# Kernel tuning notes

Measured on AMD Instinct MI355X. Metric: run time of the kernel, lower is better.

## Reference

```python
import jax, jax.numpy as jnp
import numpy as np

H = 8
DK = 32  # head_dim = 256 // 8
SCALE = 1.0 / np.float32(np.sqrt(DK))
EPS = 1e-5


def _ln(x, g, b):
    mu = jnp.mean(x, axis=-1, keepdims=True)
    var = jnp.var(x, axis=-1, keepdims=True)
    return (x - mu) / jnp.sqrt(var + EPS) * g + b


def _lin(x, W, b):
    return x @ W + b


def setup_inputs() -> dict:
    key = jax.random.key(0)
    ks = jax.random.split(key, 16)
    B, M, N, D, F = 4, 64, 512, 256, 1024
    s = 0.02
    inp = {
        "machine_emb": jax.random.normal(ks[0], (B, M, D), jnp.float32),
        "op_emb": jax.random.normal(ks[1], (B, N, D), jnp.float32),
        "edge_emb": jax.random.normal(ks[2], (B, N, M, D), jnp.float32),
        "o2m_mask": jax.random.bernoulli(ks[3], 0.3, (B, N, M)),
    }
    # projection weights stored as (in, out)
    for i, nm in enumerate(["q", "k", "v", "o", "ks", "vs", "e"]):
        inp["W" + nm] = jax.random.normal(ks[4 + i], (D, D), jnp.float32) * s
        inp["b" + nm] = jnp.zeros((D,), jnp.float32)
    # layernorms: norm1 (g1/b1), norm2 (g2/b2), norm_op (gop/bop)
    for nm in ["1", "2", "op"]:
        inp["g" + nm] = jnp.ones((D,), jnp.float32)
        inp["bn" + nm] = jnp.zeros((D,), jnp.float32)
    # FFN
    inp["Wf1"] = jax.random.normal(ks[11], (D, F), jnp.float32) * s
    inp["bf1"] = jnp.zeros((F,), jnp.float32)
    inp["Wf2"] = jax.random.normal(ks[12], (F, D), jnp.float32) * s
    inp["bf2"] = jnp.zeros((D,), jnp.float32)
    return inp


def reference(machine_emb, op_emb, edge_emb, o2m_mask,
              Wq, bq, Wk, bk, Wv, bv, Wo, bo, Wks, bks, Wvs, bvs, We, be,
              g1, bn1, g2, bn2, gop, bnop, Wf1, bf1, Wf2, bf2):
    B, M, D = machine_emb.shape
    N = op_emb.shape[1]

    residual = machine_emb
    machine_norm = _ln(machine_emb, g1, bn1)
    op_norm = _ln(op_emb, gop, bnop)

    # (B, H, M, dk) / (B, H, N, dk)
    q_m = _lin(machine_norm, Wq, bq).reshape(B, M, H, DK).transpose(0, 2, 1, 3)
    k_o = _lin(op_norm, Wk, bk).reshape(B, N, H, DK).transpose(0, 2, 1, 3)
    v_o = _lin(op_norm, Wv, bv).reshape(B, N, H, DK).transpose(0, 2, 1, 3)

    # edge: (B,N,M,D) -> (B,H,M,N,dk)
    edge = _lin(edge_emb, We, be).reshape(B, N, M, H, DK)
    edge = edge.transpose(0, 3, 2, 1, 4)  # bhmnd

    q_total = q_m[:, :, :, None, :] + edge          # (B,H,M,N,dk)
    k_total = k_o[:, :, None, :, :] + edge          # (B,H,M,N,dk)
    v_total = v_o[:, :, None, :, :] + edge          # (B,H,M,N,dk)

    scores = jnp.sum(q_total * k_total, axis=-1) * SCALE  # (B,H,M,N)

    k_self = _lin(machine_norm, Wks, bks).reshape(B, M, H, DK).transpose(0, 2, 1, 3)
    self_scores = jnp.sum(q_m * k_self, axis=-1) * SCALE   # (B,H,M)

    cross_mask = o2m_mask.transpose(0, 2, 1)[:, None, :, :]  # (B,1,M,N)
    combined_scores = jnp.concatenate([self_scores[..., None], scores], axis=-1)  # (B,H,M,1+N)
    self_flag = jnp.ones((B, 1, M, 1), dtype=bool)
    combined_mask = jnp.concatenate([self_flag, jnp.broadcast_to(cross_mask, (B, 1, M, N))], axis=-1)
    combined_scores = jnp.where(combined_mask, combined_scores, -jnp.inf)

    attn = jax.nn.softmax(combined_scores, axis=-1)
    attn = jnp.where(jnp.isnan(attn), 0.0, attn)

    v_self = _lin(machine_norm, Wvs, bvs).reshape(B, M, H, DK).transpose(0, 2, 1, 3)
    combined_values = jnp.concatenate([v_self[:, :, :, None, :], v_total], axis=3)  # (B,H,M,1+N,dk)

    attn_out = jnp.einsum('bhmi,bhmid->bhmd', attn, combined_values)
    attn_out = attn_out.transpose(0, 2, 1, 3).reshape(B, M, D)
    attn_out = _lin(attn_out, Wo, bo)

    machine_emb = residual + attn_out
    h = _ln(machine_emb, g2, bn2)
    ffn = _lin(jax.nn.relu(_lin(h, Wf1, bf1)), Wf2, bf2)
    return machine_emb + ffn
```

## Files before the change

### kernel.cpp

```cpp
#include <hip/hip_runtime.h>
#include <hip/hip_bf16.h>
#include <math.h>

#define H_ 8
#define DK_ 32
#define B_ 4
#define M_ 64
#define N_ 512
#define D_ 256
#define F_ 1024

static constexpr float SCALE = 0.17677669529663687f;
static constexpr float EPS = 1e-5f;

typedef __bf16 bf16x8 __attribute__((ext_vector_type(8)));
typedef float f32x4 __attribute__((ext_vector_type(4)));

__device__ inline float bfbits2f(unsigned int b) {
    union { unsigned int i; float f; } c; c.i = b << 16; return c.f;
}
__device__ inline void unpack8(uint4 u, float* f) {
    f[0] = bfbits2f(u.x & 0xffffu); f[1] = bfbits2f(u.x >> 16);
    f[2] = bfbits2f(u.y & 0xffffu); f[3] = bfbits2f(u.y >> 16);
    f[4] = bfbits2f(u.z & 0xffffu); f[5] = bfbits2f(u.z >> 16);
    f[6] = bfbits2f(u.w & 0xffffu); f[7] = bfbits2f(u.w >> 16);
}

__global__ __launch_bounds__(256) void detect_kernel(const unsigned int* __restrict__ mask,
                                                     int* __restrict__ flags) {
    __shared__ int s2[256];
    int t = threadIdx.x;
    int cgt = 0;
    for (int i = 0; i < 128; ++i) {
        unsigned int w = mask[t * 128 + i];
        if (w > 1u) cgt++;
    }
    s2[t] = cgt;
    __syncthreads();
    if (t == 0) {
        int b = 0;
        for (int i = 0; i < 256; ++i) b += s2[i];
        flags[1] = (b > 0) ? 1 : 0;
    }
}

struct TTArgs {
    const void* src[9];
    void* dst[9];
    int tcum[9];
    int kl[9];
    int nl[9];
};

__global__ __launch_bounds__(256) void prep_transpose(TTArgs a) {
    __shared__ float ld[64][65];
    int bx = blockIdx.x;
    int ti = 0;
    while (bx >= a.tcum[ti]) ti++;
    int j = bx - (ti ? a.tcum[ti - 1] : 0);
    int K = 1 << a.kl[ti], N = 1 << a.nl[ti];
    int ntn = N >> 6;
    int kt = j / ntn, nt = j - kt * ntn;
    const float* src = (const float*)a.src[ti];
    __hip_bfloat16* dst = (__hip_bfloat16*)a.dst[ti];
    int t = threadIdx.x;
    int col = t & 63, r0 = t >> 6;
#pragma unroll
    for (int i = 0; i < 16; ++i) {
        int r = i * 4 + r0;
        ld[r][col] = src[(size_t)(kt * 64 + r) * N + nt * 64 + col];
    }
    __syncthreads();
#pragma unroll
    for (int i = 0; i < 16; ++i) {
        int r = i * 4 + r0;
        dst[(size_t)(nt * 64 + r) * K + kt * 64 + col] = __float2bfloat16(ld[col][r]);
    }
}

__global__ __launch_bounds__(256) void prep_bias(const float* bq, const float* bks,
                                                 const float* bvs, const float* bk,
                                                 const float* bv,
                                                 float* bqksvs, float* bkv) {
    int t = threadIdx.x;
    bqksvs[t] = bq[t];
    bqksvs[256 + t] = bks[t];
    bqksvs[512 + t] = bvs[t];
    bkv[t] = bk[t];
    bkv[256 + t] = bv[t];
}

__device__ inline float block_reduce256(float v, bool is_max, float* sbuf) {
#pragma unroll
    for (int off = 32; off > 0; off >>= 1) {
        float o = __shfl_down(v, off, 64);
        v = is_max ? fmaxf(v, o) : (v + o);
    }
    int lane = threadIdx.x & 63, wid = threadIdx.x >> 6;
    if (lane == 0) sbuf[wid] = v;
    __syncthreads();
    float r;
    if (is_max) r = fmaxf(fmaxf(sbuf[0], sbuf[1]), fmaxf(sbuf[2], sbuf[3]));
    else        r = sbuf[0] + sbuf[1] + sbuf[2] + sbuf[3];
    __syncthreads();
    return r;
}

__global__ __launch_bounds__(256) void ln_kernel(const float* __restrict__ xin,
                                                 const float* __restrict__ g,
                                                 const float* __restrict__ bta,
                                                 __hip_bfloat16* __restrict__ out) {
    __shared__ float sbuf[4];
    int row = blockIdx.x, d = threadIdx.x;
    size_t idx = (size_t)row * 256 + d;
    float x = xin[idx];
    float s  = block_reduce256(x, false, sbuf);
    float ss = block_reduce256(x * x, false, sbuf);
    float mu = s * (1.f / 256.f);
    float var = ss * (1.f / 256.f) - mu * mu;
    float y = (x - mu) * rsqrtf(var + EPS) * g[d] + bta[d];
    out[idx] = __float2bfloat16(y);
}

__global__ __launch_bounds__(256) void gemm64(const __hip_bfloat16* __restrict__ A,
                                              const __hip_bfloat16* __restrict__ BT,
                                              const float* __restrict__ bias,
                                              const float* __restrict__ resid,
                                              void* __restrict__ out,
                                              int K, int ldc, int flags) {
    __shared__ __align__(16) __bf16 As[64 * 40];
    __shared__ __align__(16) __bf16 Bs[64 * 40];
    const int rowBase = blockIdx.x * 64;
    const int colBase = blockIdx.y * 64;
    const int t = threadIdx.x;
    const int w = t >> 6;
    const int l = t & 63;
    const int lrow = l & 15;
    const int lk8 = (l >> 4) * 8;
    const int ar = t >> 2;
    const int ac = (t & 3) * 8;

    f32x4 acc[4] = {};
    for (int k0 = 0; k0 < K; k0 += 32) {
        bf16x8 av = *(const bf16x8*)(A + (size_t)(rowBase + ar) * K + k0 + ac);
        bf16x8 bv = *(const bf16x8*)(BT + (size_t)(colBase + ar) * K + k0 + ac);
        __syncthreads();
        *(bf16x8*)(As + ar * 40 + ac) = av;
        *(bf16x8*)(Bs + ar * 40 + ac) = bv;
        __syncthreads();
        bf16x8 af = *(const bf16x8*)(As + (w * 16 + lrow) * 40 + lk8);
#pragma unroll
        for (int c = 0; c < 4; ++c) {
            bf16x8 bf = *(const bf16x8*)(Bs + (c * 16 + lrow) * 40 + lk8);
            acc[c] = __builtin_amdgcn_mfma_f32_16x16x32_bf16(af, bf, acc[c], 0, 0, 0);
        }
    }
    int rbase = rowBase + w * 16 + ((l >> 4) * 4);
#pragma unroll
    for (int c = 0; c < 4; ++c) {
        int col = colBase + c * 16 + (l & 15);
        float bb = bias[col];
#pragma unroll
        for (int r = 0; r < 4; ++r) {
            int row = rbase + r;
            size_t oi = (size_t)row * ldc + col;
            float v = acc[c][r] + bb;
            if (flags & 1) v = fmaxf(v, 0.f);
            if (flags & 4) v += resid[oi];
            if (flags & 8) ((float*)out)[oi] = v;
            else ((__hip_bfloat16*)out)[oi] = __float2bfloat16(v);
        }
    }
}

__global__ __launch_bounds__(256) void edge_gemm4(const float* __restrict__ E,
                                                  const __hip_bfloat16* __restrict__ WeT,
                                                  const float* __restrict__ be,
                                                  const __hip_bfloat16* __restrict__ qkvs,
                                                  const __hip_bfloat16* __restrict__ kov,
                                                  const void* __restrict__ mask,
                                                  const int* __restrict__ flags,
                                                  __hip_bfloat16* __restrict__ eperm,
                                                  float* __restrict__ scBn) {
    __shared__ __align__(16) __bf16 smem[64 * 272];
    __bf16* As = smem;
    __bf16* Cs = smem;
    const int bn = blockIdx.x;
    const int b = bn >> 9, n = bn & 511;
    const int t = threadIdx.x;
    const int w = t >> 6;
    const int l = t & 63;
    const int lrow = l & 15;
    const int lk8 = (l >> 4) * 8;
    const int ar = t >> 2;
    const int ac = (t & 3) * 8;
    const float* Ab = E + (size_t)bn * 64 * 256;

    f32x4 acc[4][4] = {};
    for (int k0 = 0; k0 < 256; k0 += 32) {
        const float* ap = Ab + (size_t)ar * 256 + k0 + ac;
        float4 x0 = *(const float4*)ap;
        float4 x1 = *(const float4*)(ap + 4);
        bf16x8 av;
        av[0] = (__bf16)x0.x; av[1] = (__bf16)x0.y; av[2] = (__bf16)x0.z; av[3] = (__bf16)x0.w;
        av[4] = (__bf16)x1.x; av[5] = (__bf16)x1.y; av[6] = (__bf16)x1.z; av[7] = (__bf16)x1.w;
        __syncthreads();
        *(bf16x8*)(As + ar * 40 + ac) = av;
        __syncthreads();
        bf16x8 af[4];
#pragma unroll
        for (int rr = 0; rr < 4; ++rr)
            af[rr] = *(const bf16x8*)(As + (rr * 16 + lrow) * 40 + lk8);
#pragma unroll
        for (int c = 0; c < 4; ++c) {
            bf16x8 bf = *(const bf16x8*)(WeT + (size_t)(w * 64 + c * 16 + lrow) * 256 + k0 + lk8);
#pragma unroll
            for (int rr = 0; rr < 4; ++rr)
                acc[rr][c] = __builtin_amdgcn_mfma_f32_16x16x32_bf16(af[rr], bf, acc[rr][c], 0, 0, 0);
        }
    }
    __syncthreads();
#pragma unroll
    for (int c = 0; c < 4; ++c) {
        int col = w * 64 + c * 16 + (l & 15);
        float bb = be[col];
#pragma unroll
        for (int rr = 0; rr < 4; ++rr) {
#pragma unroll
            for (int r = 0; r < 4; ++r) {
                int m = rr * 16 + (l >> 4) * 4 + r;
                Cs[m * 272 + col] = (__bf16)(acc[rr][c][r] + bb);
            }
        }
    }
    __syncthreads();
    const bool u8 = flags[1] != 0;
    const int seg = t & 31;
    const int h = seg >> 2;
    const int dk8 = (seg & 3) * 8;
#pragma unroll
    for (int j = 0; j < 8; ++j) {
        int m = j * 8 + (t >> 5);
        uint4 ev4 = *(const uint4*)(Cs + m * 272 + seg * 8);
        size_t bhm = (size_t)((b * 8 + h) * 64 + m);
        *(uint4*)(eperm + (bhm * 512 + n) * 32 + dk8) = ev4;
        float ev[8], qf[8], kf[8];
        unpack8(ev4, ev);
        uint4 qv4 = *(const uint4*)(qkvs + (size_t)(b * 64 + m) * 768 + h * 32 + dk8);
        uint4 kv4 = *(const uint4*)(kov + (size_t)(b * 512 + n) * 512 + h * 32 + dk8);
        unpack8(qv4, qf);
        unpack8(kv4, kf);
        float p = 0.f;
#pragma unroll
        for (int i = 0; i < 8; ++i)
            p += (qf[i] + ev[i]) * (kf[i] + ev[i]);
        p += __shfl_xor(p, 1, 64);
        p += __shfl_xor(p, 2, 64);
        if ((t & 3) == 0) {
            int mi = (b * 512 + n) * 64 + m;
            int mk = u8 ? (int)((const unsigned char*)mask)[mi] : ((const int*)mask)[mi];
            scBn[(size_t)bn * 512 + h * 64 + m] = mk ? p * SCALE : -__builtin_inff();
        }
    }
}

__global__ __launch_bounds__(256) void transpose_sc(const float* __restrict__ in,
                                                    float* __restrict__ out) {
    __shared__ float ld[64][65];
    int b = blockIdx.z;
    int n0 = blockIdx.x * 64;
    int hm0 = blockIdx.y * 64;
    int t = threadIdx.x;
    int col = t & 63, r0 = t >> 6;
#pragma unroll
    for (int i = 0; i < 16; ++i) {
        int r = i * 4 + r0;
        ld[r][col] = in[((size_t)(b * 512 + n0 + r)) * 512 + hm0 + col];
    }
    __syncthreads();
#pragma unroll
    for (int i = 0; i < 16; ++i) {
        int r = i * 4 + r0;
        out[((size_t)(b * 512 + hm0 + r)) * 512 + n0 + col] = ld[col][r];
    }
}

__global__ __launch_bounds__(256) void smax_attnout(const float* __restrict__ sc,
                                                    const __hip_bfloat16* __restrict__ qkvs,
                                                    const __hip_bfloat16* __restrict__ kov,
                                                    const __hip_bfloat16* __restrict__ eperm,
                                                    __hip_bfloat16* __restrict__ AO) {
    __shared__ float sbuf[4];
    __shared__ float attnS[512];
    __shared__ float selfSc;
    __shared__ float selfA;
    __shared__ float red[16][8];
    int bhm = blockIdx.x;
    int m = bhm & 63;
    int h = (bhm >> 6) & 7;
    int b = bhm >> 9;
    int t = threadIdx.x;
    if (t == 0) {
        const __hip_bfloat16* q  = qkvs + (size_t)(b * 64 + m) * 768 + h * 32;
        const __hip_bfloat16* ks = q + 256;
        float s = 0.f;
        for (int i = 0; i < 32; ++i) s += __bfloat162float(q[i]) * __bfloat162float(ks[i]);
        selfSc = s * SCALE;
    }
    __syncthreads();
    float sv = selfSc;
    float s0 = sc[(size_t)bhm * 512 + t];
    float s1 = sc[(size_t)bhm * 512 + 256 + t];
    float mx = block_reduce256(fmaxf(fmaxf(s0, s1), sv), true, sbuf);
    float e0 = __expf(s0 - mx);
    float e1 = __expf(s1 - mx);
    float eself = __expf(sv - mx);
    float sum = block_reduce256(e0 + e1 + (t == 0 ? eself : 0.f), false, sbuf);
    float inv = 1.f / sum;
    attnS[t] = e0 * inv;
    attnS[256 + t] = e1 * inv;
    if (t == 0) selfA = eself * inv;
    __syncthreads();

    const int d8 = (t & 3) * 8;
    const int ng = t >> 2;
    const int w = t >> 6, l = t & 63;
    const __hip_bfloat16* ebase = eperm + (size_t)bhm * 512 * 32;
    const __hip_bfloat16* vbase = kov + (size_t)(b * 512) * 512 + 256 + h * 32;
    float accv[8] = {};
#pragma unroll
    for (int i = 0; i < 8; ++i) {
        int n = ng + i * 64;
        float a = attnS[n];
        float ev[8], vv[8];
        uint4 e4 = *(const uint4*)(ebase + (size_t)n * 32 + d8);
        uint4 v4 = *(const uint4*)(vbase + (size_t)n * 512 + d8);
        unpack8(e4, ev);
        unpack8(v4, vv);
#pragma unroll
        for (int k = 0; k < 8; ++k) accv[k] += a * (vv[k] + ev[k]);
    }
#pragma unroll
    for (int off = 4; off <= 32; off <<= 1) {
#pragma unroll
        for (int k = 0; k < 8; ++k) accv[k] += __shfl_xor(accv[k], off, 64);
    }
    if ((l >> 2) == 0) {
#pragma unroll
        for (int k = 0; k < 8; ++k) red[w * 4 + (l & 3)][k] = accv[k];
    }
    __syncthreads();
    if (t < 32) {
        int slot = t >> 3, elem = t & 7;
        float r = red[slot][elem] + red[4 + slot][elem] + red[8 + slot][elem] + red[12 + slot][elem];
        float vs = __bfloat162float(qkvs[(size_t)(b * 64 + m) * 768 + 512 + h * 32 + t]);
        r += selfA * vs;
        AO[(size_t)(b * 64 + m) * 256 + h * 32 + t] = __float2bfloat16(r);
    }
}

extern "C" void kernel_launch(void* const* d_in, const int* in_sizes, int n_in,
                              void* d_out, int out_size, void* d_ws, size_t ws_size,
                              hipStream_t stream) {
    const float* machine_emb = (const float*)d_in[0];
    const float* op_emb      = (const float*)d_in[1];
    const float* edge_emb    = (const float*)d_in[2];
    const void*  o2m_mask    = d_in[3];

    char* p = (char*)d_ws;
    int* flags = (int*)p;                        p += 256;
    __hip_bfloat16* WqksvsT = (__hip_bfloat16*)p; p += 196608 * 2;
    __hip_bfloat16* WkvT    = (__hip_bfloat16*)p; p += 131072 * 2;
    __hip_bfloat16* WoT     = (__hip_bfloat16*)p; p += 65536 * 2;
    __hip_bfloat16* WeT     = (__hip_bfloat16*)p; p += 65536 * 2;
    __hip_bfloat16* Wf1T    = (__hip_bfloat16*)p; p += 262144 * 2;
    __hip_bfloat16* Wf2T    = (__hip_bfloat16*)p; p += 262144 * 2;
    float* bqksvs           = (float*)p;          p += 768 * 4;
    float* bkv              = (float*)p;          p += 512 * 4;
    __hip_bfloat16* mnorm   = (__hip_bfloat16*)p; p += 65536 * 2;
    __hip_bfloat16* onorm   = (__hip_bfloat16*)p; p += 524288 * 2;
    __hip_bfloat16* qkvs    = (__hip_bfloat16*)p; p += 196608 * 2;
    __hip_bfloat16* kov     = (__hip_bfloat16*)p; p += 1048576 * 2;
    __hip_bfloat16* eperm   = (__hip_bfloat16*)p; p += (size_t)33554432 * 2;
    float* scBn      = (float*)p;                p += (size_t)1048576 * 4;
    float* scT       = (float*)p;                p += (size_t)1048576 * 4;
    __hip_bfloat16* AO = (__hip_bfloat16*)p;     p += 65536 * 2;
    float* m2        = (float*)p;                p += 65536 * 4;
    __hip_bfloat16* hn = (__hip_bfloat16*)p;     p += 65536 * 2;
    __hip_bfloat16* h1 = (__hip_bfloat16*)p;     p += 262144 * 2;

    TTArgs ta;
    const int srcIdx[9] = {4, 12, 14, 6, 8, 10, 16, 24, 26};
    void* dsts[9] = {WqksvsT, WqksvsT + 65536, WqksvsT + 131072,
                     WkvT, WkvT + 65536, WoT, WeT, Wf1T, Wf2T};
    const int kl9[9] = {8, 8, 8, 8, 8, 8, 8, 8, 10};
    const int nl9[9] = {8, 8, 8, 8, 8, 8, 8, 10, 8};
    int tcum = 0;
    for (int i = 0; i < 9; ++i) {
        ta.src[i] = d_in[srcIdx[i]];
        ta.dst[i] = dsts[i];
        int tiles = (1 << (kl9[i] - 6)) * (1 << (nl9[i] - 6));
        tcum += tiles;
        ta.tcum[i] = tcum;
        ta.kl[i] = kl9[i];
        ta.nl[i] = nl9[i];
    }

    hipLaunchKernelGGL(detect_kernel, dim3(1), dim3(256), 0, stream,
                       (const unsigned int*)o2m_mask, flags);
    hipLaunchKernelGGL(prep_transpose, dim3(tcum), dim3(256), 0, stream, ta);
    hipLaunchKernelGGL(prep_bias, dim3(1), dim3(256), 0, stream,
                       (const float*)d_in[5], (const float*)d_in[13],
                       (const float*)d_in[15], (const float*)d_in[7],
                       (const float*)d_in[9], bqksvs, bkv);

    hipLaunchKernelGGL(ln_kernel, dim3(256), dim3(256), 0, stream,
                       machine_emb, (const float*)d_in[18], (const float*)d_in[19], mnorm);
    hipLaunchKernelGGL(ln_kernel, dim3(2048), dim3(256), 0, stream,
                       op_emb, (const float*)d_in[22], (const float*)d_in[23], onorm);

    hipLaunchKernelGGL(gemm64, dim3(4, 12), dim3(256), 0, stream,
                       mnorm, WqksvsT, bqksvs, nullptr, qkvs, 256, 768, 0);
    hipLaunchKernelGGL(gemm64, dim3(32, 8), dim3(256), 0, stream,
                       onorm, WkvT, bkv, nullptr, kov, 256, 512, 0);

    hipLaunchKernelGGL(edge_gemm4, dim3(2048), dim3(256), 0, stream,
                       edge_emb, WeT, (const float*)d_in[17],
                       qkvs, kov, o2m_mask, flags, eperm, scBn);

    hipLaunchKernelGGL(transpose_sc, dim3(8, 8, 4), dim3(256), 0, stream, scBn, scT);

    hipLaunchKernelGGL(smax_attnout, dim3(2048), dim3(256), 0, stream,
                       scT, qkvs, kov, eperm, AO);

    hipLaunchKernelGGL(gemm64, dim3(4, 4), dim3(256), 0, stream,
                       AO, WoT, (const float*)d_in[11], machine_emb, m2, 256, 256, 4 | 8);
    hipLaunchKernelGGL(ln_kernel, dim3(256), dim3(256), 0, stream,
                       m2, (const float*)d_in[20], (const float*)d_in[21], hn);
    hipLaunchKernelGGL(gemm64, dim3(4, 16), dim3(256), 0, stream,
                       hn, Wf1T, (const float*)d_in[25], nullptr, h1, 256, 1024, 1);
    hipLaunchKernelGGL(gemm64, dim3(4, 4), dim3(256), 0, stream,
                       h1, Wf2T, (const float*)d_in[27], m2, (float*)d_out, 1024, 256, 4 | 8);
}
```

Before: 382.2 us.

## Halve edge GEMM epilogue LDS via two-pass staging to raise occupancy

The edge projection kernel's epilogue now stages the output tile through shared memory in two half-width passes, halving LDS use per block. A launch bound asks for 8 blocks per CU so more waves can overlap the large fp32 edge stream. Each thread's k vector is also loaded once per pass instead of once per row. The cost is an extra barrier pass and possible register pressure under the tighter launch bound.

```diff
diff --git a/kernel.cpp b/kernel.cpp
--- a/kernel.cpp
+++ b/kernel.cpp
@@ -173,16 +173,16 @@
     }
 }
 
-__global__ __launch_bounds__(256) void edge_gemm4(const float* __restrict__ E,
-                                                  const __hip_bfloat16* __restrict__ WeT,
-                                                  const float* __restrict__ be,
-                                                  const __hip_bfloat16* __restrict__ qkvs,
-                                                  const __hip_bfloat16* __restrict__ kov,
-                                                  const void* __restrict__ mask,
-                                                  const int* __restrict__ flags,
-                                                  __hip_bfloat16* __restrict__ eperm,
-                                                  float* __restrict__ scBn) {
-    __shared__ __align__(16) __bf16 smem[64 * 272];
+__global__ __launch_bounds__(256, 8) void edge_gemm5(const float* __restrict__ E,
+                                                     const __hip_bfloat16* __restrict__ WeT,
+                                                     const float* __restrict__ be,
+                                                     const __hip_bfloat16* __restrict__ qkvs,
+                                                     const __hip_bfloat16* __restrict__ kov,
+                                                     const void* __restrict__ mask,
+                                                     const int* __restrict__ flags,
+                                                     __hip_bfloat16* __restrict__ eperm,
+                                                     float* __restrict__ scBn) {
+    __shared__ __align__(16) __bf16 smem[64 * 136];
     __bf16* As = smem;
     __bf16* Cs = smem;
     const int bn = blockIdx.x;
@@ -219,47 +219,54 @@
                 acc[rr][c] = __builtin_amdgcn_mfma_f32_16x16x32_bf16(af[rr], bf, acc[rr][c], 0, 0, 0);
         }
     }
-    __syncthreads();
-#pragma unroll
-    for (int c = 0; c < 4; ++c) {
-        int col = w * 64 + c * 16 + (l & 15);
-        float bb = be[col];
-#pragma unroll
-        for (int rr = 0; rr < 4; ++rr) {
-#pragma unroll
-            for (int r = 0; r < 4; ++r) {
-                int m = rr * 16 + (l >> 4) * 4 + r;
-                Cs[m * 272 + col] = (__bf16)(acc[rr][c][r] + bb);
+    const bool u8 = flags[1] != 0;
+#pragma unroll
+    for (int pass = 0; pass < 2; ++pass) {
+        __syncthreads();
+#pragma unroll
+        for (int c2 = 0; c2 < 2; ++c2) {
+            int c = pass * 2 + c2;
+            int col = w * 64 + c * 16 + (l & 15);
+            int pc = w * 32 + c2 * 16 + (l & 15);
+            float bb = be[col];
+#pragma unroll
+            for (int rr = 0; rr < 4; ++rr) {
+#pragma unroll
+                for (int r = 0; r < 4; ++r) {
+                    int m = rr * 16 + (l >> 4) * 4 + r;
+                    Cs[m * 136 + pc] = (__bf16)(acc[rr][c][r] + bb);
+                }
             }
         }
-    }
-    __syncthreads();
-    const bool u8 = flags[1] != 0;
-    const int seg = t & 31;
-    const int h = seg >> 2;
-    const int dk8 = (seg & 3) * 8;
-#pragma unroll
-    for (int j = 0; j < 8; ++j) {
-        int m = j * 8 + (t >> 5);
-        uint4 ev4 = *(const uint4*)(Cs + m * 272 + seg * 8);
-        size_t bhm = (size_t)((b * 8 + h) * 64 + m);
-        *(uint4*)(eperm + (bhm * 512 + n) * 32 + dk8) = ev4;
-        float ev[8], qf[8], kf[8];
-        unpack8(ev4, ev);
-        uint4 qv4 = *(const uint4*)(qkvs + (size_t)(b * 64 + m) * 768 + h * 32 + dk8);
-        uint4 kv4 = *(const uint4*)(kov + (size_t)(b * 512 + n) * 512 + h * 32 + dk8);
-        unpack8(qv4, qf);
+        __syncthreads();
+        const int u = t & 15;
+        const int pci8 = u * 8;
+        const int hh = (pci8 >> 5) * 2 + pass;
+        const int dk8 = pci8 & 31;
+        float kf[8];
+        uint4 kv4 = *(const uint4*)(kov + (size_t)(b * 512 + n) * 512 + hh * 32 + dk8);
         unpack8(kv4, kf);
-        float p = 0.f;
-#pragma unroll
-        for (int i = 0; i < 8; ++i)
-            p += (qf[i] + ev[i]) * (kf[i] + ev[i]);
-        p += __shfl_xor(p, 1, 64);
-        p += __shfl_xor(p, 2, 64);
-        if ((t & 3) == 0) {
-            int mi = (b * 512 + n) * 64 + m;
-            int mk = u8 ? (int)((const unsigned char*)mask)[mi] : ((const int*)mask)[mi];
-            scBn[(size_t)bn * 512 + h * 64 + m] = mk ? p * SCALE : -__builtin_inff();
+#pragma unroll
+        for (int j = 0; j < 4; ++j) {
+            int m = j * 16 + (t >> 4);
+            uint4 ev4 = *(const uint4*)(Cs + m * 136 + pci8);
+            size_t bhm = (size_t)((b * 8 + hh) * 64 + m);
+            *(uint4*)(eperm + (bhm * 512 + n) * 32 + dk8) = ev4;
+            float ev[8], qf[8];
+            unpack8(ev4, ev);
+            uint4 qv4 = *(const uint4*)(qkvs + (size_t)(b * 64 + m) * 768 + hh * 32 + dk8);
+            unpack8(qv4, qf);
+            float p = 0.f;
+#pragma unroll
+            for (int i = 0; i < 8; ++i)
+                p += (qf[i] + ev[i]) * (kf[i] + ev[i]);
+            p += __shfl_xor(p, 1, 64);
+            p += __shfl_xor(p, 2, 64);
+            if ((t & 3) == 0) {
+                int mi = (b * 512 + n) * 64 + m;
+                int mk = u8 ? (int)((const unsigned char*)mask)[mi] : ((const int*)mask)[mi];
+                scBn[(size_t)bn * 512 + hh * 64 + m] = mk ? p * SCALE : -__builtin_inff();
+            }
         }
     }
 }
@@ -424,7 +431,7 @@
     hipLaunchKernelGGL(gemm64, dim3(32, 8), dim3(256), 0, stream,
                        onorm, WkvT, bkv, nullptr, kov, 256, 512, 0);
 
-    hipLaunchKernelGGL(edge_gemm4, dim3(2048), dim3(256), 0, stream,
+    hipLaunchKernelGGL(edge_gemm5, dim3(2048), dim3(256), 0, stream,
                        edge_emb, WeT, (const float*)d_in[17],
                        qkvs, kov, o2m_mask, flags, eperm, scBn);
 
```

Measured after the change: 656.9 us. +71.9%, slower.
